# Optimization experiments

Measured on AMD Instinct MI355X. Metric: run time of the kernel, lower is better.

Reference implementation:

```python
import jax, jax.numpy as jnp
import numpy as np

H = 16      # num_attention_heads
HKV = 4     # num_key_value_heads
HIDDEN = 1024
HEAD_DIM = HIDDEN // H  # 64
ROPE_BASE = 10000.0


def _rope(x):
    # Rotate-half RoPE applied over the FULL projected last dim, matching the
    # module which applies self._rope before splitting into heads.
    B, S, D = x.shape
    half = D // 2
    inv_freq = 1.0 / (ROPE_BASE ** (jnp.arange(half, dtype=jnp.float32) / half))
    ang = jnp.arange(S, dtype=jnp.float32)[:, None] * inv_freq[None, :]  # [S, half]
    cos, sin = jnp.cos(ang), jnp.sin(ang)
    x1, x2 = x[..., :half], x[..., half:]
    return jnp.concatenate([x1 * cos - x2 * sin, x2 * cos + x1 * sin], axis=-1)


def _rmsnorm(x):
    # F.rms_norm with no weight: x / sqrt(mean(x^2) + eps)
    eps = jnp.finfo(x.dtype).eps
    return x * jax.lax.rsqrt(jnp.mean(x * x, axis=-1, keepdims=True) + eps)


def setup_inputs() -> dict:
    key = jax.random.key(0)
    ks = jax.random.split(key, 10)
    B, S = 2, 2048
    kv_dim = HKV * HEAD_DIM
    sc = 0.02
    return {
        "hidden_state": jax.random.normal(ks[0], (B, S, HIDDEN), dtype=jnp.float32),
        "attention_mask": jnp.zeros((B, S, S), dtype=jnp.float32),
        "Wq": jax.random.normal(ks[1], (HIDDEN, HIDDEN), dtype=jnp.float32) * sc,
        "bq": jnp.zeros((HIDDEN,), dtype=jnp.float32),
        "Wk": jax.random.normal(ks[2], (HIDDEN, kv_dim), dtype=jnp.float32) * sc,
        "bk": jnp.zeros((kv_dim,), dtype=jnp.float32),
        "Wv": jax.random.normal(ks[3], (HIDDEN, kv_dim), dtype=jnp.float32) * sc,
        "bv": jnp.zeros((kv_dim,), dtype=jnp.float32),
        "Wo": jax.random.normal(ks[4], (HIDDEN, HIDDEN), dtype=jnp.float32) * sc,
        "bo": jnp.zeros((HIDDEN,), dtype=jnp.float32),
    }


def reference(hidden_state, attention_mask, Wq, bq, Wk, bk, Wv, bv, Wo, bo):
    B, S, _ = hidden_state.shape
    G = H // HKV  # query heads per kv head
    d = HEAD_DIM

    q = hidden_state @ Wq + bq            # [B,S,H*d]
    k = hidden_state @ Wk + bk            # [B,S,Hkv*d]
    v = hidden_state @ Wv + bv            # [B,S,Hkv*d]

    q = _rope(q)
    k = _rope(k)

    # split heads; repeat_interleave of KV over groups == grouping Q heads as [Hkv, G]
    q = q.reshape(B, S, H, d).transpose(0, 2, 1, 3).reshape(B, HKV, G, S, d)
    k = k.reshape(B, S, HKV, d).transpose(0, 2, 1, 3)   # [B,Hkv,S,d]
    v = v.reshape(B, S, HKV, d).transpose(0, 2, 1, 3)   # [B,Hkv,S,d]

    q = _rmsnorm(q)
    k = _rmsnorm(k)

    scale = d ** 0.5
    scores = jnp.einsum('bkgqd,bksd->bkgqs', q, k) / scale  # [B,Hkv,G,S,S]
    scores = scores + attention_mask[:, None, None, :, :]
    attn = jax.nn.softmax(scores, axis=-1)
    out = jnp.einsum('bkgqs,bksd->bkgqd', attn, v)          # [B,Hkv,G,S,d]

    out = out.reshape(B, H, S, d).transpose(0, 2, 1, 3).reshape(B, S, H * d)
    return out @ Wo + bo
```

## Files before the change

### kernel.cpp

```cpp
#include <hip/hip_runtime.h>
#include <cmath>

#define SEQ 2048
#define BATCH 2
#define HID 1024
#define NH 16
#define NKV 4
#define DH 64
#define KVDIM 256
#define K32C 32

typedef __attribute__((ext_vector_type(8))) short bf16x8;
typedef __attribute__((ext_vector_type(4))) float f32x4;

static __device__ __forceinline__ unsigned short f2bf(float x) {
  union { float f; unsigned u; } v; v.f = x;
  unsigned r = v.u + 0x7fffu + ((v.u >> 16) & 1u);
  return (unsigned short)(r >> 16);
}
static __device__ __forceinline__ float bf2f(unsigned short h) {
  union { unsigned u; float f; } v; v.u = ((unsigned)h) << 16;
  return v.f;
}
static __device__ __forceinline__ void gl_lds16(const void* g, void* l) {
  __builtin_amdgcn_global_load_lds(
      (const __attribute__((address_space(1))) unsigned int*)g,
      (__attribute__((address_space(3))) unsigned int*)l, 16, 0, 0);
}

template<bool HILO>
__global__ __launch_bounds__(256) void pack_a_kernel(
    const float* __restrict__ A, unsigned short* __restrict__ hi,
    unsigned short* __restrict__ lo) {
  int gid = blockIdx.x * 256 + threadIdx.x;
  int lane = gid & 63;
  int k32 = (gid >> 6) & 31;
  int m16 = gid >> 11;
  int quad = lane >> 4, l16 = lane & 15;
  const float* src = A + (size_t)(m16 * 16 + l16) * 1024 + k32 * 32 + quad * 8;
  float4 a0 = *(const float4*)src;
  float4 a1 = *(const float4*)(src + 4);
  float v[8] = {a0.x, a0.y, a0.z, a0.w, a1.x, a1.y, a1.z, a1.w};
  unsigned short h[8], l[8];
#pragma unroll
  for (int j = 0; j < 8; ++j) {
    h[j] = f2bf(v[j]);
    if (HILO) l[j] = f2bf(v[j] - bf2f(h[j]));
  }
  *(bf16x8*)(hi + (size_t)gid * 8) = *(bf16x8*)h;
  if (HILO) *(bf16x8*)(lo + (size_t)gid * 8) = *(bf16x8*)l;
}

template<bool HILO>
__global__ __launch_bounds__(256) void pack_b_kernel(
    const float* __restrict__ W, unsigned short* __restrict__ hi,
    unsigned short* __restrict__ lo, int Nsrc) {
  int gid = blockIdx.x * 256 + threadIdx.x;
  int lane = gid & 63;
  int k32 = (gid >> 6) & 31;
  int n16 = gid >> 11;
  int quad = lane >> 4, l16 = lane & 15;
  int n = n16 * 16 + l16, k = k32 * 32 + quad * 8;
  unsigned short h[8], l[8];
#pragma unroll
  for (int j = 0; j < 8; ++j) {
    float v = W[(size_t)(k + j) * Nsrc + n];
    h[j] = f2bf(v);
    if (HILO) l[j] = f2bf(v - bf2f(h[j]));
  }
  *(bf16x8*)(hi + (size_t)gid * 8) = *(bf16x8*)h;
  if (HILO) *(bf16x8*)(lo + (size_t)gid * 8) = *(bf16x8*)l;
}

__global__ __launch_bounds__(256) void bias_cat_kernel(
    const float* __restrict__ bq, const float* __restrict__ bk,
    const float* __restrict__ bv, float* __restrict__ dst) {
  int n = blockIdx.x * 256 + threadIdx.x;
  if (n < 1536)
    dst[n] = (n < 1024) ? bq[n] : (n < 1280 ? bk[n - 1024] : bv[n - 1280]);
}

template<int CHAINS, bool OUTBF16>
__global__ __launch_bounds__(256) void gemm_pk_kernel(
    const unsigned short* __restrict__ Ah, const unsigned short* __restrict__ Al,
    const unsigned short* __restrict__ Bh, const unsigned short* __restrict__ Bl,
    const float* __restrict__ bias, void* __restrict__ Cout, int N) {
  constexpr int NCH = (CHAINS == 3) ? 2 : 1;
  __shared__ unsigned short Asm[NCH][4 * 512];
  __shared__ unsigned short Bsm[NCH][8 * 512];
  const int tid = threadIdx.x;
  const int wave = tid >> 6, lane = tid & 63;
  const int wr = wave >> 1, wc = wave & 1;
  const int quad = lane >> 4, l16 = lane & 15;
  const size_t abase = ((size_t)(blockIdx.y * 4 + wave) * K32C) * 64 + lane;
  const size_t bbase0 = ((size_t)(blockIdx.x * 8 + wave) * K32C) * 64 + lane;
  const size_t bbase1 = ((size_t)(blockIdx.x * 8 + wave + 4) * K32C) * 64 + lane;
  f32x4 acc[2][4] = {};
  for (int k32 = 0; k32 < K32C; ++k32) {
    __syncthreads();
    gl_lds16(Ah + (abase + (size_t)k32 * 64) * 8, &Asm[0][wave * 512]);
    gl_lds16(Bh + (bbase0 + (size_t)k32 * 64) * 8, &Bsm[0][wave * 512]);
    gl_lds16(Bh + (bbase1 + (size_t)k32 * 64) * 8, &Bsm[0][(wave + 4) * 512]);
    if (CHAINS == 3) {
      gl_lds16(Al + (abase + (size_t)k32 * 64) * 8, &Asm[1][wave * 512]);
      gl_lds16(Bl + (bbase0 + (size_t)k32 * 64) * 8, &Bsm[1][wave * 512]);
      gl_lds16(Bl + (bbase1 + (size_t)k32 * 64) * 8, &Bsm[1][(wave + 4) * 512]);
    }
    __syncthreads();
    bf16x8 af[2][NCH], bfr[4][NCH];
#pragma unroll
    for (int mt = 0; mt < 2; ++mt)
#pragma unroll
      for (int ch = 0; ch < NCH; ++ch)
        af[mt][ch] = *(const bf16x8*)&Asm[ch][((wr * 2 + mt) * 64 + lane) * 8];
#pragma unroll
    for (int nt = 0; nt < 4; ++nt)
#pragma unroll
      for (int ch = 0; ch < NCH; ++ch)
        bfr[nt][ch] = *(const bf16x8*)&Bsm[ch][((wc * 4 + nt) * 64 + lane) * 8];
#pragma unroll
    for (int mt = 0; mt < 2; ++mt)
#pragma unroll
      for (int nt = 0; nt < 4; ++nt) {
        acc[mt][nt] = __builtin_amdgcn_mfma_f32_16x16x32_bf16(af[mt][0], bfr[nt][0], acc[mt][nt], 0, 0, 0);
        if (CHAINS == 3) {
          acc[mt][nt] = __builtin_amdgcn_mfma_f32_16x16x32_bf16(af[mt][1], bfr[nt][0], acc[mt][nt], 0, 0, 0);
          acc[mt][nt] = __builtin_amdgcn_mfma_f32_16x16x32_bf16(af[mt][0], bfr[nt][1], acc[mt][nt], 0, 0, 0);
        }
      }
  }
  const int n0 = blockIdx.x * 128 + wc * 64;
  const int m0 = blockIdx.y * 64 + wr * 32;
#pragma unroll
  for (int mt = 0; mt < 2; ++mt)
#pragma unroll
    for (int nt = 0; nt < 4; ++nt)
#pragma unroll
      for (int r = 0; r < 4; ++r) {
        int gm = m0 + mt * 16 + quad * 4 + r;
        int n = n0 + nt * 16 + l16;
        float v = acc[mt][nt][r] + bias[n];
        if (OUTBF16)
          ((unsigned short*)Cout)[(size_t)gm * N + n] = f2bf(v);
        else
          ((float*)Cout)[(size_t)gm * N + n] = v;
      }
}

__global__ __launch_bounds__(1024) void rope_norm_q_kernel(
    const unsigned short* __restrict__ qkv, unsigned short* __restrict__ Qh,
    unsigned short* __restrict__ Ql) {
  const int s = blockIdx.x, b = blockIdx.y;
  const int t = threadIdx.x;
  const unsigned short* row = qkv + ((size_t)b * SEQ + s) * 1536;
  const int j = t & 511;
  float invf = exp2f((float)j * (-13.287712379549449f / 512.0f));
  float ang = (float)s * invf;
  float c = cosf(ang), sn = sinf(ang);
  float x1 = bf2f(row[j]), x2 = bf2f(row[j + 512]);
  float val = (t < 512) ? (x1 * c - x2 * sn) : (x2 * c + x1 * sn);
  float ss = val * val;
#pragma unroll
  for (int off = 1; off < 64; off <<= 1) ss += __shfl_xor(ss, off);
  float rn = rsqrtf(ss * (1.0f / 64.0f) + 1.1920929e-07f);
  float v = val * rn;
  unsigned short hi = f2bf(v);
  unsigned short lo = f2bf(v - bf2f(hi));
  int h = t >> 6, d = t & 63;
  size_t o = (size_t)(b * NH + h) * 131072 +
             ((((size_t)(s >> 4) * 2 + (d >> 5)) * 64) + ((d >> 3) & 3) * 16 + (s & 15)) * 8 + (d & 7);
  Qh[o] = hi;
  Ql[o] = lo;
}

__global__ __launch_bounds__(256) void rope_norm_kv_kernel(
    const unsigned short* __restrict__ qkv, unsigned short* __restrict__ Kpk,
    unsigned short* __restrict__ Vpk) {
  const int s = blockIdx.x, b = blockIdx.y;
  const int t = threadIdx.x;
  const unsigned short* row = qkv + ((size_t)b * SEQ + s) * 1536;
  const int j = t & 127;
  float invf = exp2f((float)j * (-13.287712379549449f / 128.0f));
  float ang = (float)s * invf;
  float c = cosf(ang), sn = sinf(ang);
  float x1 = bf2f(row[1024 + j]), x2 = bf2f(row[1024 + 128 + j]);
  float val = (t < 128) ? (x1 * c - x2 * sn) : (x2 * c + x1 * sn);
  float ss = val * val;
#pragma unroll
  for (int off = 1; off < 64; off <<= 1) ss += __shfl_xor(ss, off);
  float rn = rsqrtf(ss * (1.0f / 64.0f) + 1.1920929e-07f);
  float kv = val * rn;
  int h = t >> 6, d = t & 63;
  size_t ko = (size_t)(b * NKV + h) * 131072 +
              ((((size_t)(s >> 4) * 2 + (d >> 5)) * 64) + ((d >> 3) & 3) * 16 + (s & 15)) * 8 + (d & 7);
  Kpk[ko] = f2bf(kv);
  size_t vo = (size_t)(b * NKV + h) * 131072 +
              ((((size_t)(d >> 4) * 64 + (s >> 5)) * 64) + ((s >> 3) & 3) * 16 + (d & 15)) * 8 + (s & 7);
  Vpk[vo] = row[1280 + t];
}

__global__ __launch_bounds__(512, 4) void attn_mfma6_kernel(
    const unsigned short* __restrict__ Qh, const unsigned short* __restrict__ Ql,
    const unsigned short* __restrict__ Kpk, const unsigned short* __restrict__ Vpk,
    const float* __restrict__ mask, float* __restrict__ attn_o) {
  __shared__ __align__(16) char smem[67584];
  unsigned short* Kb = (unsigned short*)smem;
  unsigned short* Vb = (unsigned short*)(smem + 16384);
  float*          Msk = (float*)(smem + 32768);
  unsigned short* Ps = (unsigned short*)(smem + 49152);

  const int b = blockIdx.z, kvh = blockIdx.y;
  const int q0 = blockIdx.x * 32;
  const int tid = threadIdx.x, wave = tid >> 6, lane = tid & 63;
  const int jh = wave >> 2, w4 = wave & 3;
  const int quad = lane >> 4, l16 = lane & 15;
  const int h = kvh * 4 + w4;

  bf16x8 qh[2][2], ql[2][2];
  {
    const unsigned short* Qb_h = Qh + (size_t)(b * NH + h) * 131072;
    const unsigned short* Qb_l = Ql + (size_t)(b * NH + h) * 131072;
#pragma unroll
    for (int mt = 0; mt < 2; ++mt)
#pragma unroll
      for (int kf = 0; kf < 2; ++kf) {
        size_t o = ((((size_t)(q0 >> 4) + mt) * 2 + kf) * 64 + lane) * 8;
        qh[mt][kf] = *(const bf16x8*)(Qb_h + o);
        ql[mt][kf] = *(const bf16x8*)(Qb_l + o);
      }
  }

  const unsigned short* Kbase = Kpk + (size_t)(b * NKV + kvh) * 131072;
  const unsigned short* Vbase = Vpk + (size_t)(b * NKV + kvh) * 131072;

  const float* mbase = mask + ((size_t)b * SEQ + q0) * SEQ;
  const int srow = w4 * 8 + (lane >> 3);
  const int ssw = ((srow >> 2) & 1) << 4;
  const float* msrc0 = mbase + (size_t)srow * SEQ + (((lane & 7) * 4) ^ ssw);

  bf16x8 ones;
#pragma unroll
  for (int i = 0; i < 8; ++i) ones[i] = (short)0x3F80;

  f32x4 O[2][4] = {};
  f32x4 lAcc[2] = {};

  auto stage = [&](int buf, int jc) {
    const int j0 = jh * (SEQ / 2) + jc * 32;
    gl_lds16(Kbase + ((((size_t)(j0 >> 4) + (w4 >> 1)) * 2 + (w4 & 1)) * 64 + lane) * 8,
             Kb + (buf * 2 + jh) * 2048 + w4 * 512);
    gl_lds16(Vbase + (((size_t)w4 * 64 + (j0 >> 5)) * 64 + lane) * 8,
             Vb + (buf * 2 + jh) * 2048 + w4 * 512);
    gl_lds16(msrc0 + j0, Msk + (buf * 2 + jh) * 1024 + w4 * 256);
  };

  stage(0, 0);
  for (int jc = 0; jc < 32; ++jc) {
    const int cur = jc & 1;
    __syncthreads();
    if (jc < 31) stage(cur ^ 1, jc + 1);

    bf16x8 kbf[2][2], vbf[4];
#pragma unroll
    for (int nt = 0; nt < 2; ++nt)
#pragma unroll
      for (int kf = 0; kf < 2; ++kf)
        kbf[nt][kf] = *(const bf16x8*)&Kb[(cur * 2 + jh) * 2048 + ((nt * 2 + kf) * 64 + lane) * 8];
#pragma unroll
    for (int d16 = 0; d16 < 4; ++d16)
      vbf[d16] = *(const bf16x8*)&Vb[(cur * 2 + jh) * 2048 + (d16 * 64 + lane) * 8];

    bf16x8 pa[2];
#pragma unroll
    for (int mt = 0; mt < 2; ++mt) {
#pragma unroll
      for (int nt = 0; nt < 2; ++nt) {
        f32x4 C = {};
        C = __builtin_amdgcn_mfma_f32_16x16x32_bf16(qh[mt][0], kbf[nt][0], C, 0, 0, 0);
        C = __builtin_amdgcn_mfma_f32_16x16x32_bf16(qh[mt][1], kbf[nt][1], C, 0, 0, 0);
        C = __builtin_amdgcn_mfma_f32_16x16x32_bf16(ql[mt][0], kbf[nt][0], C, 0, 0, 0);
        C = __builtin_amdgcn_mfma_f32_16x16x32_bf16(ql[mt][1], kbf[nt][1], C, 0, 0, 0);
#pragma unroll
        for (int r = 0; r < 4; ++r) {
          int row16 = quad * 4 + r;
          float m = Msk[(cur * 2 + jh) * 1024 + (mt * 16 + row16) * 32 +
                        ((nt * 16 + l16) ^ ((quad & 1) << 4))];
          float p = __builtin_amdgcn_exp2f(
              fmaf(C[r], 0.18033688f, fmaf(m, 1.44269504f, -11.54156033f)));
          union { float f; unsigned u; } pu; pu.f = p;
          Ps[wave * 1152 + row16 * 72 + nt * 16 + l16] =
              (unsigned short)((pu.u + 0x8000u) >> 16);
        }
      }
      pa[mt] = *(const bf16x8*)&Ps[wave * 1152 + l16 * 72 + quad * 8];
    }
#pragma unroll
    for (int mt = 0; mt < 2; ++mt) {
      lAcc[mt] = __builtin_amdgcn_mfma_f32_16x16x32_bf16(pa[mt], ones, lAcc[mt], 0, 0, 0);
#pragma unroll
      for (int nt = 0; nt < 4; ++nt)
        O[mt][nt] = __builtin_amdgcn_mfma_f32_16x16x32_bf16(pa[mt], vbf[nt], O[mt][nt], 0, 0, 0);
    }
  }

  __syncthreads();
  float* Oex = (float*)smem;
  float* lex = (float*)(smem + 34816);
  if (jh == 1) {
#pragma unroll
    for (int mt = 0; mt < 2; ++mt)
#pragma unroll
      for (int r = 0; r < 4; ++r) {
        int row = mt * 16 + quad * 4 + r;
#pragma unroll
        for (int nt = 0; nt < 4; ++nt)
          Oex[((size_t)w4 * 32 + row) * 68 + nt * 16 + l16] = O[mt][nt][r];
        if (l16 == 0) lex[w4 * 32 + row] = lAcc[mt][r];
      }
  }
  __syncthreads();
  if (jh == 0) {
    float* po = attn_o + ((size_t)b * SEQ + q0) * HID + h * DH;
#pragma unroll
    for (int mt = 0; mt < 2; ++mt)
#pragma unroll
      for (int r = 0; r < 4; ++r) {
        int row = mt * 16 + quad * 4 + r;
        float inv = 1.0f / (lAcc[mt][r] + lex[w4 * 32 + row]);
#pragma unroll
        for (int nt = 0; nt < 4; ++nt) {
          float v = (O[mt][nt][r] + Oex[((size_t)w4 * 32 + row) * 68 + nt * 16 + l16]) * inv;
          po[(size_t)row * HID + nt * 16 + l16] = v;
        }
      }
  }
}

extern "C" void kernel_launch(void* const* d_in, const int* in_sizes, int n_in,
                              void* d_out, int out_size, void* d_ws, size_t ws_size,
                              hipStream_t stream) {
  const float* hs   = (const float*)d_in[0];
  const float* mask = (const float*)d_in[1];
  const float* Wq   = (const float*)d_in[2];
  const float* bq   = (const float*)d_in[3];
  const float* Wk   = (const float*)d_in[4];
  const float* bk   = (const float*)d_in[5];
  const float* Wv   = (const float*)d_in[6];
  const float* bv   = (const float*)d_in[7];
  const float* Wo   = (const float*)d_in[8];
  const float* bo   = (const float*)d_in[9];
  float* out = (float*)d_out;
  char* ws = (char*)d_ws;
  const size_t MiB = 1048576;

  unsigned short* hs_pk   = (unsigned short*)(ws);
  unsigned short* qkvproj = (unsigned short*)(ws + 8 * MiB);
  float*          attn_o  = (float*)(ws);
  unsigned short* Wqkv_hi = (unsigned short*)(ws + 20 * MiB);
  unsigned short* Wo_hi   = (unsigned short*)(ws + 20 * MiB);
  unsigned short* Wo_lo   = (unsigned short*)(ws + 22 * MiB);
  unsigned short* Qpk_h   = (unsigned short*)(ws + 24 * MiB);
  unsigned short* Qpk_l   = (unsigned short*)(ws + 32 * MiB);
  unsigned short* ao_hi   = (unsigned short*)(ws + 24 * MiB);
  unsigned short* ao_lo   = (unsigned short*)(ws + 32 * MiB);
  unsigned short* Kpk     = (unsigned short*)(ws + 40 * MiB);
  unsigned short* Vpk     = (unsigned short*)(ws + 42 * MiB);
  float*          bias_c  = (float*)(ws + 44 * MiB);

  pack_a_kernel<false><<<2048, 256, 0, stream>>>(hs, hs_pk, nullptr);
  pack_b_kernel<false><<<512, 256, 0, stream>>>(Wq, Wqkv_hi, nullptr, 1024);
  pack_b_kernel<false><<<128, 256, 0, stream>>>(Wk, Wqkv_hi + (size_t)64 * 2048 * 8, nullptr, 256);
  pack_b_kernel<false><<<128, 256, 0, stream>>>(Wv, Wqkv_hi + (size_t)80 * 2048 * 8, nullptr, 256);
  bias_cat_kernel<<<6, 256, 0, stream>>>(bq, bk, bv, bias_c);

  gemm_pk_kernel<1, true><<<dim3(12, 64), 256, 0, stream>>>(
      hs_pk, nullptr, Wqkv_hi, nullptr, bias_c, qkvproj, 1536);

  pack_b_kernel<true><<<512, 256, 0, stream>>>(Wo, Wo_hi, Wo_lo, 1024);

  rope_norm_q_kernel<<<dim3(SEQ, BATCH), dim3(1024), 0, stream>>>(qkvproj, Qpk_h, Qpk_l);
  rope_norm_kv_kernel<<<dim3(SEQ, BATCH), dim3(256), 0, stream>>>(qkvproj, Kpk, Vpk);

  attn_mfma6_kernel<<<dim3(SEQ / 32, NKV, BATCH), dim3(512), 0, stream>>>(
      Qpk_h, Qpk_l, Kpk, Vpk, mask, attn_o);

  pack_a_kernel<true><<<2048, 256, 0, stream>>>(attn_o, ao_hi, ao_lo);
  gemm_pk_kernel<3, false><<<dim3(8, 64), 256, 0, stream>>>(
      ao_hi, ao_lo, Wo_hi, Wo_lo, bo, out, 1024);
}
```

Baseline: 270.6 us.

## Enlarge GEMM tiles to 128x128 and double-buffer LDS staging

Grows the packed GEMM block tile from 64x128 to 128x128, so each wave computes a 4x4 grid of MFMA tiles and gets more reuse from each LDS load. It also double-buffers the LDS stages, issuing the next k-slice's global-to-LDS copies before computing on the current one, and drops one barrier per iteration. Both the QKV and output projections use the new kernel, at half the grid size in M. The trade-off is more registers and LDS per block and fewer blocks on the GPU, which could reduce occupancy.

```diff
diff --git a/kernel.cpp b/kernel.cpp
--- a/kernel.cpp
+++ b/kernel.cpp
@@ -81,45 +81,53 @@
 }
 
 template<int CHAINS, bool OUTBF16>
-__global__ __launch_bounds__(256) void gemm_pk_kernel(
+__global__ __launch_bounds__(256, 2) void gemm_pk128_kernel(
     const unsigned short* __restrict__ Ah, const unsigned short* __restrict__ Al,
     const unsigned short* __restrict__ Bh, const unsigned short* __restrict__ Bl,
     const float* __restrict__ bias, void* __restrict__ Cout, int N) {
   constexpr int NCH = (CHAINS == 3) ? 2 : 1;
-  __shared__ unsigned short Asm[NCH][4 * 512];
-  __shared__ unsigned short Bsm[NCH][8 * 512];
+  __shared__ unsigned short Asm[2][NCH][8 * 512];
+  __shared__ unsigned short Bsm[2][NCH][8 * 512];
   const int tid = threadIdx.x;
   const int wave = tid >> 6, lane = tid & 63;
   const int wr = wave >> 1, wc = wave & 1;
   const int quad = lane >> 4, l16 = lane & 15;
-  const size_t abase = ((size_t)(blockIdx.y * 4 + wave) * K32C) * 64 + lane;
-  const size_t bbase0 = ((size_t)(blockIdx.x * 8 + wave) * K32C) * 64 + lane;
-  const size_t bbase1 = ((size_t)(blockIdx.x * 8 + wave + 4) * K32C) * 64 + lane;
-  f32x4 acc[2][4] = {};
+
+  auto stage = [&](int buf, int k32) {
+#pragma unroll
+    for (int i = 0; i < 2; ++i) {
+      int c = wave * 2 + i;
+      size_t asrc = (((size_t)(blockIdx.y * 8 + c) * K32C + k32) * 64 + lane) * 8;
+      size_t bsrc = (((size_t)(blockIdx.x * 8 + c) * K32C + k32) * 64 + lane) * 8;
+      gl_lds16(Ah + asrc, &Asm[buf][0][c * 512]);
+      gl_lds16(Bh + bsrc, &Bsm[buf][0][c * 512]);
+      if (CHAINS == 3) {
+        gl_lds16(Al + asrc, &Asm[buf][1][c * 512]);
+        gl_lds16(Bl + bsrc, &Bsm[buf][1][c * 512]);
+      }
+    }
+  };
+
+  f32x4 acc[4][4] = {};
+  stage(0, 0);
   for (int k32 = 0; k32 < K32C; ++k32) {
+    const int cur = k32 & 1;
     __syncthreads();
-    gl_lds16(Ah + (abase + (size_t)k32 * 64) * 8, &Asm[0][wave * 512]);
-    gl_lds16(Bh + (bbase0 + (size_t)k32 * 64) * 8, &Bsm[0][wave * 512]);
-    gl_lds16(Bh + (bbase1 + (size_t)k32 * 64) * 8, &Bsm[0][(wave + 4) * 512]);
-    if (CHAINS == 3) {
-      gl_lds16(Al + (abase + (size_t)k32 * 64) * 8, &Asm[1][wave * 512]);
-      gl_lds16(Bl + (bbase0 + (size_t)k32 * 64) * 8, &Bsm[1][wave * 512]);
-      gl_lds16(Bl + (bbase1 + (size_t)k32 * 64) * 8, &Bsm[1][(wave + 4) * 512]);
-    }
-    __syncthreads();
-    bf16x8 af[2][NCH], bfr[4][NCH];
-#pragma unroll
-    for (int mt = 0; mt < 2; ++mt)
+    if (k32 < K32C - 1) stage(cur ^ 1, k32 + 1);
+
+    bf16x8 af[4][NCH], bfr[4][NCH];
+#pragma unroll
+    for (int mt = 0; mt < 4; ++mt)
 #pragma unroll
       for (int ch = 0; ch < NCH; ++ch)
-        af[mt][ch] = *(const bf16x8*)&Asm[ch][((wr * 2 + mt) * 64 + lane) * 8];
+        af[mt][ch] = *(const bf16x8*)&Asm[cur][ch][((wr * 4 + mt) * 64 + lane) * 8];
 #pragma unroll
     for (int nt = 0; nt < 4; ++nt)
 #pragma unroll
       for (int ch = 0; ch < NCH; ++ch)
-        bfr[nt][ch] = *(const bf16x8*)&Bsm[ch][((wc * 4 + nt) * 64 + lane) * 8];
-#pragma unroll
-    for (int mt = 0; mt < 2; ++mt)
+        bfr[nt][ch] = *(const bf16x8*)&Bsm[cur][ch][((wc * 4 + nt) * 64 + lane) * 8];
+#pragma unroll
+    for (int mt = 0; mt < 4; ++mt)
 #pragma unroll
       for (int nt = 0; nt < 4; ++nt) {
         acc[mt][nt] = __builtin_amdgcn_mfma_f32_16x16x32_bf16(af[mt][0], bfr[nt][0], acc[mt][nt], 0, 0, 0);
@@ -129,10 +137,10 @@
         }
       }
   }
+  const int m0 = blockIdx.y * 128 + wr * 64;
   const int n0 = blockIdx.x * 128 + wc * 64;
-  const int m0 = blockIdx.y * 64 + wr * 32;
-#pragma unroll
-  for (int mt = 0; mt < 2; ++mt)
+#pragma unroll
+  for (int mt = 0; mt < 4; ++mt)
 #pragma unroll
     for (int nt = 0; nt < 4; ++nt)
 #pragma unroll
@@ -373,7 +381,7 @@
   pack_b_kernel<false><<<128, 256, 0, stream>>>(Wv, Wqkv_hi + (size_t)80 * 2048 * 8, nullptr, 256);
   bias_cat_kernel<<<6, 256, 0, stream>>>(bq, bk, bv, bias_c);
 
-  gemm_pk_kernel<1, true><<<dim3(12, 64), 256, 0, stream>>>(
+  gemm_pk128_kernel<1, true><<<dim3(12, 32), 256, 0, stream>>>(
       hs_pk, nullptr, Wqkv_hi, nullptr, bias_c, qkvproj, 1536);
 
   pack_b_kernel<true><<<512, 256, 0, stream>>>(Wo, Wo_hi, Wo_lo, 1024);
@@ -385,6 +393,6 @@
       Qpk_h, Qpk_l, Kpk, Vpk, mask, attn_o);
 
   pack_a_kernel<true><<<2048, 256, 0, stream>>>(attn_o, ao_hi, ao_lo);
-  gemm_pk_kernel<3, false><<<dim3(8, 64), 256, 0, stream>>>(
+  gemm_pk128_kernel<3, false><<<dim3(8, 32), 256, 0, stream>>>(
       ao_hi, ao_lo, Wo_hi, Wo_lo, bo, out, 1024);
 }
```

Result: slower. 285.9 us (+5.7%).
